# Kernel optimization log

Measured on AMD Instinct MI355X. Metric: run time of the kernel, lower is better.

## Reference

```python
import jax, jax.numpy as jnp
import numpy as np

TEMPERATURE = 0.07
EPS = 1e-12  # F.normalize clamp


def _project(x, We, be, W1, b1, W2, b2):
    # encoder Linear then projection head Linear->ReLU->Linear
    h = x @ We + be                      # [B, 512]
    h = jax.nn.relu(h @ W1 + b1)         # [B, 256]
    return h @ W2 + b2                   # [B, 128]


def _ntxent(z1, z2, t):
    B = z1.shape[0]
    z1 = z1 / jnp.maximum(jnp.linalg.norm(z1, axis=1, keepdims=True), EPS)
    z2 = z2 / jnp.maximum(jnp.linalg.norm(z2, axis=1, keepdims=True), EPS)
    reps = jnp.concatenate([z1, z2], axis=0)          # [2B, 128]
    sim = reps @ reps.T                               # [2B, 2B]
    N = 2 * B
    idx = jnp.arange(N)
    # positives: eye rolled by B along columns -> column (i+B) mod N
    pos = sim[idx, (idx + B) % N][:, None]            # [N, 1]
    # negatives: all off-diagonal entries per row, in column order
    cols = jnp.arange(N - 1)[None, :]                 # [1, N-1]
    neg_idx = cols + (cols >= idx[:, None])           # skip the diagonal
    neg = jnp.take_along_axis(sim, neg_idx, axis=1)   # [N, N-1]
    logits = jnp.concatenate([pos, neg], axis=1) / t  # [N, N]
    # cross-entropy with label 0
    return jnp.mean(jax.nn.logsumexp(logits, axis=1) - logits[:, 0])


def setup_inputs() -> dict:
    key = jax.random.key(0)
    ks = jax.random.split(key, 10)
    B, Din, Denc, Dh, Dp = 4096, 1024, 512, 256, 128
    s = lambda fan_in: 1.0 / np.sqrt(fan_in)
    return {
        "x_image": jax.random.normal(ks[0], (B, Din), jnp.float32),
        "x_text": jax.random.normal(ks[1], (B, Din), jnp.float32),
        "We_img": jax.random.normal(ks[2], (Din, Denc), jnp.float32) * s(Din),
        "be_img": jnp.zeros((Denc,), jnp.float32),
        "We_txt": jax.random.normal(ks[3], (Din, Denc), jnp.float32) * s(Din),
        "be_txt": jnp.zeros((Denc,), jnp.float32),
        "Wp1_img": jax.random.normal(ks[4], (Denc, Dh), jnp.float32) * s(Denc),
        "bp1_img": jnp.zeros((Dh,), jnp.float32),
        "Wp2_img": jax.random.normal(ks[5], (Dh, Dp), jnp.float32) * s(Dh),
        "bp2_img": jnp.zeros((Dp,), jnp.float32),
        "Wp1_txt": jax.random.normal(ks[6], (Denc, Dh), jnp.float32) * s(Denc),
        "bp1_txt": jnp.zeros((Dh,), jnp.float32),
        "Wp2_txt": jax.random.normal(ks[7], (Dh, Dp), jnp.float32) * s(Dh),
        "bp2_txt": jnp.zeros((Dp,), jnp.float32),
    }


def reference(x_image, x_text, We_img, be_img, We_txt, be_txt,
              Wp1_img, bp1_img, Wp2_img, bp2_img,
              Wp1_txt, bp1_txt, Wp2_txt, bp2_txt):
    z1 = _project(x_image, We_img, be_img, Wp1_img, bp1_img, Wp2_img, bp2_img)
    z2 = _project(x_text, We_txt, be_txt, Wp1_txt, bp1_txt, Wp2_txt, bp2_txt)
    # single modality pair ('image','text') -> one NT-Xent loss
    return _ntxent(z1, z2, TEMPERATURE)
```

## Files before the change

kernel.cpp:

```cpp
#include <hip/hip_runtime.h>
#include <hip/hip_bf16.h>
#include <math.h>

typedef __bf16 bf16_t;
typedef __bf16 bf8 __attribute__((ext_vector_type(8)));
typedef __bf16 bf4 __attribute__((ext_vector_type(4)));
typedef float f32x4 __attribute__((ext_vector_type(4)));
typedef int i32x8 __attribute__((ext_vector_type(8)));
typedef unsigned char u8;

#define AS1 __attribute__((address_space(1)))
#define AS3 __attribute__((address_space(3)))

#define B_ROWS 4096
#define NTOT   8192
#define DIN    1024
#define DENC   512
#define DH     256
#define DP     128
#define NSLICE 64
#define INV_T        14.285714285714286f
#define SCALE_LOG2   20.609929155556620f

__device__ __forceinline__ f32x4 mfma_16x16x32(bf8 a, bf8 b, f32x4 c) {
  return __builtin_amdgcn_mfma_f32_16x16x32_bf16(a, b, c, 0, 0, 0);
}

__global__ __launch_bounds__(256) void prep_kernel(
    const float* __restrict__ x_i, const float* __restrict__ x_t,
    const float* __restrict__ We_i, const float* __restrict__ We_t,
    const float* __restrict__ W1_i, const float* __restrict__ W1_t,
    const float* __restrict__ W2_i, const float* __restrict__ W2_t,
    bf16_t* __restrict__ xb_i, bf16_t* __restrict__ xb_t,
    bf16_t* __restrict__ Wet_i, bf16_t* __restrict__ Wet_t,
    bf16_t* __restrict__ W1t_i, bf16_t* __restrict__ W1t_t,
    bf16_t* __restrict__ W2t_i, bf16_t* __restrict__ W2t_t) {
  const int b = blockIdx.x;
  const int tid = threadIdx.x;
  if (b >= 336) {
    int idx = (b - 336) * 256 + tid;
    const int HALF = (B_ROWS * DIN) / 4;
    const float* s; bf16_t* d; int off;
    if (idx < HALF) { s = x_i; d = xb_i; off = idx; }
    else            { s = x_t; d = xb_t; off = idx - HALF; }
    float4 v = ((const float4*)s)[off];
    bf4 w = { (bf16_t)v.x, (bf16_t)v.y, (bf16_t)v.z, (bf16_t)v.w };
    ((bf4*)d)[off] = w;
    return;
  }
  const float* src; bf16_t* dst; int K, N, tile;
  if (b < 128)      { src = We_i; dst = Wet_i; K = 1024; N = 512; tile = b; }
  else if (b < 256) { src = We_t; dst = Wet_t; K = 1024; N = 512; tile = b - 128; }
  else if (b < 288) { src = W1_i; dst = W1t_i; K = 512;  N = 256; tile = b - 256; }
  else if (b < 320) { src = W1_t; dst = W1t_t; K = 512;  N = 256; tile = b - 288; }
  else if (b < 328) { src = W2_i; dst = W2t_i; K = 256;  N = 128; tile = b - 320; }
  else              { src = W2_t; dst = W2t_t; K = 256;  N = 128; tile = b - 328; }
  const int tilesN = N >> 6;
  const int k0 = (tile / tilesN) * 64;
  const int n0 = (tile % tilesN) * 64;

  __shared__ float ld[64][65];
  #pragma unroll
  for (int i = 0; i < 4; ++i) {
    int cid = tid + i * 256;
    int r = cid >> 4;
    int c = (cid & 15) * 4;
    float4 v = *(const float4*)(src + (size_t)(k0 + r) * N + n0 + c);
    ld[r][c + 0] = v.x; ld[r][c + 1] = v.y; ld[r][c + 2] = v.z; ld[r][c + 3] = v.w;
  }
  __syncthreads();
  #pragma unroll
  for (int i = 0; i < 2; ++i) {
    int cid = tid + i * 256;
    int rn = cid >> 3;
    int c8 = (cid & 7) * 8;
    bf8 w;
    #pragma unroll
    for (int j = 0; j < 8; ++j) w[j] = (bf16_t)ld[c8 + j][rn];
    *(bf8*)(dst + (size_t)(n0 + rn) * K + k0 + c8) = w;
  }
}

template<int MT, bool RELU>
__global__ __launch_bounds__(256) void gemm_glds(
    const bf16_t* __restrict__ A0, const bf16_t* __restrict__ A1,
    const bf16_t* __restrict__ B0, const bf16_t* __restrict__ B1,
    const float* __restrict__ bias0, const float* __restrict__ bias1,
    bf16_t* __restrict__ out0, bf16_t* __restrict__ out1,
    int N, int K) {
  const bf16_t* A   = blockIdx.z ? A1 : A0;
  const bf16_t* Bt  = blockIdx.z ? B1 : B0;
  const float* bias = blockIdx.z ? bias1 : bias0;
  bf16_t* outp      = blockIdx.z ? out1 : out0;

  const int nb   = blockIdx.x * 64;
  const int mb   = blockIdx.y * MT;
  const int tid  = threadIdx.x;
  const int wave = tid >> 6;
  const int lane = tid & 63;
  const int l15  = lane & 15;
  const int quad = lane >> 4;
  constexpr int CH = MT / 64;

  __shared__ __align__(16) bf16_t As[2][MT * 32];
  __shared__ __align__(16) bf16_t Bs[2][64 * 32];

  f32x4 acc[CH][4];
  #pragma unroll
  for (int i = 0; i < CH; ++i)
    #pragma unroll
    for (int j = 0; j < 4; ++j) acc[i][j] = (f32x4){0.f, 0.f, 0.f, 0.f};

  auto stage = [&](int k0, int pb) {
    #pragma unroll
    for (int i = 0; i < CH; ++i) {
      const int s = tid + i * 256;
      const bf16_t* ga = A + (size_t)(mb + (s >> 2)) * K + k0 + (s & 3) * 8;
      __builtin_amdgcn_global_load_lds(
          (const AS1 void*)ga,
          (AS3 void*)(As[pb] + (size_t)(wave * 64 + i * 256) * 8), 16, 0, 0);
    }
    const bf16_t* gb = Bt + (size_t)(nb + (tid >> 2)) * K + k0 + (tid & 3) * 8;
    __builtin_amdgcn_global_load_lds(
        (const AS1 void*)gb,
        (AS3 void*)(Bs[pb] + (size_t)(wave * 64) * 8), 16, 0, 0);
  };

  stage(0, 0);
  const int T = K >> 5;
  for (int t = 0; t < T; ++t) {
    __syncthreads();
    if (t + 1 < T) stage((t + 1) << 5, (t + 1) & 1);
    const bf16_t* as = As[t & 1];
    const bf16_t* bs = Bs[t & 1];
    bf8 a[CH];
    #pragma unroll
    for (int i = 0; i < CH; ++i)
      a[i] = *(const bf8*)(as + (size_t)(wave * (16 * CH) + i * 16 + l15) * 32 + quad * 8);
    #pragma unroll
    for (int nt = 0; nt < 4; ++nt) {
      bf8 bb = *(const bf8*)(bs + (size_t)(nt * 16 + l15) * 32 + quad * 8);
      #pragma unroll
      for (int i = 0; i < CH; ++i)
        acc[i][nt] = mfma_16x16x32(a[i], bb, acc[i][nt]);
    }
  }

  #pragma unroll
  for (int i = 0; i < CH; ++i) {
    const int orow = mb + wave * (16 * CH) + i * 16 + quad * 4;
    #pragma unroll
    for (int nt = 0; nt < 4; ++nt) {
      const int ocol = nb + nt * 16 + l15;
      const float bval = bias[ocol];
      #pragma unroll
      for (int r = 0; r < 4; ++r) {
        float v = acc[i][nt][r] + bval;
        if (RELU) v = fmaxf(v, 0.f);
        outp[(size_t)(orow + r) * N + ocol] = (bf16_t)v;
      }
    }
  }
}

__global__ __launch_bounds__(256) void head2_norm(
    const bf16_t* __restrict__ A0, const bf16_t* __restrict__ A1,
    const bf16_t* __restrict__ B0, const bf16_t* __restrict__ B1,
    const float* __restrict__ bias0, const float* __restrict__ bias1,
    u8* __restrict__ reps8) {
  const bf16_t* A   = blockIdx.z ? A1 : A0;
  const bf16_t* Bt  = blockIdx.z ? B1 : B0;
  const float* bias = blockIdx.z ? bias1 : bias0;

  const int mb   = blockIdx.x * 16;
  const int tid  = threadIdx.x;
  const int wave = tid >> 6;
  const int lane = tid & 63;
  const int l15  = lane & 15;
  const int quad = lane >> 4;
  const int wc0  = wave * 32;

  __shared__ __align__(16) bf16_t Asb[2][16 * 32];
  __shared__ __align__(16) bf16_t Bsb[2][128 * 32];
  __shared__ float ssL[64];

  f32x4 acc[2];
  acc[0] = (f32x4){0.f, 0.f, 0.f, 0.f};
  acc[1] = (f32x4){0.f, 0.f, 0.f, 0.f};

  auto stage = [&](int k0, int pb) {
    if (wave == 0) {
      const int row = lane >> 2, j = lane & 3, cf = j ^ (row & 3);
      const bf16_t* ga = A + (size_t)(mb + row) * DH + k0 + cf * 8;
      __builtin_amdgcn_global_load_lds(
          (const AS1 void*)ga, (AS3 void*)(Asb[pb]), 16, 0, 0);
    }
    #pragma unroll
    for (int i = 0; i < 2; ++i) {
      const int s = wave * 64 + i * 256 + lane;
      const int col = s >> 2, j = s & 3, cf = j ^ (col & 3);
      const bf16_t* gb = Bt + (size_t)col * DH + k0 + cf * 8;
      __builtin_amdgcn_global_load_lds(
          (const AS1 void*)gb,
          (AS3 void*)(Bsb[pb] + (size_t)(wave * 64 + i * 256) * 8), 16, 0, 0);
    }
  };

  stage(0, 0);
  for (int t = 0; t < 8; ++t) {
    __syncthreads();
    if (t < 7) stage((t + 1) << 5, (t + 1) & 1);
    const bf16_t* as = Asb[t & 1];
    const bf16_t* bs = Bsb[t & 1];
    bf8 a = *(const bf8*)(as + (size_t)(l15 * 4 + (quad ^ (l15 & 3))) * 8);
    #pragma unroll
    for (int nt = 0; nt < 2; ++nt) {
      const int col = wc0 + nt * 16 + l15;
      bf8 bb = *(const bf8*)(bs + (size_t)(col * 4 + (quad ^ (col & 3))) * 8);
      acc[nt] = mfma_16x16x32(a, bb, acc[nt]);
    }
  }

  float ssp[4];
  #pragma unroll
  for (int r = 0; r < 4; ++r) {
    #pragma unroll
    for (int nt = 0; nt < 2; ++nt) acc[nt][r] += bias[wc0 + nt * 16 + l15];
    float s = acc[0][r] * acc[0][r] + acc[1][r] * acc[1][r];
    s += __shfl_xor(s, 1); s += __shfl_xor(s, 2);
    s += __shfl_xor(s, 4); s += __shfl_xor(s, 8);
    ssp[r] = s;
  }
  if (l15 == 0) {
    #pragma unroll
    for (int r = 0; r < 4; ++r) ssL[wave * 16 + quad * 4 + r] = ssp[r];
  }
  __syncthreads();
  const size_t gr0 = (size_t)(blockIdx.z ? B_ROWS : 0) + mb + quad * 4;
  #pragma unroll
  for (int r = 0; r < 4; ++r) {
    const int row = quad * 4 + r;
    float tot = ssL[row] + ssL[16 + row] + ssL[32 + row] + ssL[48 + row];
    const float inv = 1.0f / fmaxf(sqrtf(tot), 1e-12f);
    int pk = __builtin_amdgcn_cvt_pk_fp8_f32(acc[0][r] * inv, acc[1][r] * inv, 0, 0);
    reps8[(gr0 + r) * DP + wc0 + l15]      = (u8)(pk & 0xff);
    reps8[(gr0 + r) * DP + wc0 + 16 + l15] = (u8)((pk >> 8) & 0xff);
  }
}

__global__ __launch_bounds__(256, 4) void sim_fp8_kernel(
    const u8* __restrict__ reps8, float* __restrict__ Spart) {
  const int l = blockIdx.x;
  int by = (int)((65.0f - sqrtf(4225.0f - 4.0f * (float)l)) * 0.5f);
  while ((by + 1) * (65 - (by + 1)) <= l) ++by;
  while (by * (65 - by) > l) --by;
  const int bxh = 2 * by + (l - by * (65 - by));
  const bool diag = (bxh - 2 * by) < 2;
  const int rowbase = by * 256;
  const int col0    = bxh * 128;
  const int tid  = threadIdx.x;
  const int wave = tid >> 6;
  const int lane = tid & 63;
  const int l15  = lane & 15;
  const int quad = lane >> 4;

  __shared__ __align__(16) u8 Bs[2][64 * DP];
  __shared__ float csw[4][128];

  const int r0 = rowbase + wave * 64;
  i32x8 af[4];
  #pragma unroll
  for (int c = 0; c < 4; ++c) {
    const uint4* ap = (const uint4*)(reps8 + (size_t)(r0 + c * 16 + l15) * DP + quad * 32);
    uint4 x0 = ap[0], x1 = ap[1];
    af[c] = (i32x8){(int)x0.x, (int)x0.y, (int)x0.z, (int)x0.w,
                    (int)x1.x, (int)x1.y, (int)x1.z, (int)x1.w};
  }

  float rs[4][4];
  #pragma unroll
  for (int c = 0; c < 4; ++c)
    #pragma unroll
    for (int r = 0; r < 4; ++r) rs[c][r] = 0.f;

  auto stage = [&](int t, int pb) {
    const int jt0 = col0 + t * 64;
    #pragma unroll
    for (int i = 0; i < 2; ++i) {
      const int s   = i * 256 + tid;
      const int col = s >> 3;
      const int cf  = (s & 7) ^ (col & 7);
      const u8* g = reps8 + (size_t)(jt0 + col) * DP + cf * 16;
      __builtin_amdgcn_global_load_lds(
          (const AS1 void*)g,
          (AS3 void*)(Bs[pb] + (size_t)(i * 256 + wave * 64) * 16), 16, 0, 0);
    }
  };

  stage(0, 0);
  for (int t = 0; t < 2; ++t) {
    __syncthreads();
    if (t == 0) stage(1, 1);
    const u8* buf = Bs[t & 1];

    #pragma unroll
    for (int g = 0; g < 2; ++g) {
      f32x4 pacc[2][4];
      __builtin_amdgcn_s_setprio(1);
      #pragma unroll
      for (int h = 0; h < 2; ++h) {
        const int st = g * 2 + h;
        const int coln = st * 16 + l15;
        const u8* cbase = buf + (size_t)coln * DP;
        const int c0 = ((2 * quad)     ^ (coln & 7)) * 16;
        const int c1 = ((2 * quad + 1) ^ (coln & 7)) * 16;
        uint4 b0 = *(const uint4*)(cbase + c0);
        uint4 b1 = *(const uint4*)(cbase + c1);
        i32x8 bf = (i32x8){(int)b0.x, (int)b0.y, (int)b0.z, (int)b0.w,
                           (int)b1.x, (int)b1.y, (int)b1.z, (int)b1.w};
        #pragma unroll
        for (int c = 0; c < 4; ++c) {
          pacc[h][c] = __builtin_amdgcn_mfma_scale_f32_16x16x128_f8f6f4(
              af[c], bf, (f32x4){0.f, 0.f, 0.f, 0.f}, 0, 0, 0,
              0x7F7F7F7F, 0, 0x7F7F7F7F);
        }
      }
      __builtin_amdgcn_s_setprio(0);

      #pragma unroll
      for (int h = 0; h < 2; ++h) {
        float csp[4] = {0.f, 0.f, 0.f, 0.f};
        #pragma unroll
        for (int c = 0; c < 4; ++c) {
          #pragma unroll
          for (int r = 0; r < 4; ++r) {
            float ev = __builtin_amdgcn_exp2f(pacc[h][c][r] * SCALE_LOG2);
            rs[c][r] += ev;
            csp[r] += ev;
          }
        }
        if (!diag) {
          float cs = (csp[0] + csp[1]) + (csp[2] + csp[3]);
          cs += __shfl_xor(cs, 16);
          cs += __shfl_xor(cs, 32);
          if (quad == 0) csw[wave][t * 64 + (g * 2 + h) * 16 + l15] = cs;
        }
      }
    }
  }

  #pragma unroll
  for (int c = 0; c < 4; ++c) {
    const int i0 = r0 + c * 16 + quad * 4;
    #pragma unroll
    for (int r = 0; r < 4; ++r) {
      float v = rs[c][r];
      v += __shfl_xor(v, 1); v += __shfl_xor(v, 2);
      v += __shfl_xor(v, 4); v += __shfl_xor(v, 8);
      if (l15 == 0) Spart[(size_t)bxh * NTOT + i0 + r] = v;
    }
  }

  if (!diag) {
    __syncthreads();
    if (tid < 128) {
      Spart[(size_t)(2 * by) * NTOT + col0 + tid] = csw[0][tid] + csw[1][tid];
    } else {
      const int j = tid - 128;
      Spart[(size_t)(2 * by + 1) * NTOT + col0 + j] = csw[2][j] + csw[3][j];
    }
  }
}

__global__ __launch_bounds__(256) void rowfinal_kernel(
    const u8* __restrict__ reps8, const float* __restrict__ Spart,
    float* __restrict__ L) {
  const int tid  = threadIdx.x;
  const int wave = tid >> 6;
  const int lane = tid & 63;
  const int row  = blockIdx.x * 4 + wave;
  const int ua = *(const unsigned short*)(reps8 + (size_t)row * DP + lane * 2);
  const int ub = *(const unsigned short*)(reps8 + (size_t)(row ^ B_ROWS) * DP + lane * 2);
  float a0 = __builtin_amdgcn_cvt_f32_fp8(ua, 0);
  float a1 = __builtin_amdgcn_cvt_f32_fp8(ua, 1);
  float b0 = __builtin_amdgcn_cvt_f32_fp8(ub, 0);
  float b1 = __builtin_amdgcn_cvt_f32_fp8(ub, 1);
  float dii = a0 * a0 + a1 * a1;
  float pos = a0 * b0 + a1 * b1;
  float ps  = Spart[(size_t)lane * NTOT + row];
  #pragma unroll
  for (int m = 1; m < 64; m <<= 1) {
    dii += __shfl_xor(dii, m);
    pos += __shfl_xor(pos, m);
    ps  += __shfl_xor(ps, m);
  }
  if (lane == 0) {
    float Si = ps - __builtin_amdgcn_exp2f(dii * SCALE_LOG2)
                  + __builtin_amdgcn_exp2f(pos * SCALE_LOG2);
    L[row] = logf(Si) - pos * INV_T;
  }
}

__global__ __launch_bounds__(1024) void reduce_kernel(
    const float* __restrict__ L, float* __restrict__ out) {
  const int tid = threadIdx.x;
  float acc = 0.f;
  for (int i = tid; i < NTOT; i += 1024) acc += L[i];
  #pragma unroll
  for (int m = 1; m < 64; m <<= 1) acc += __shfl_xor(acc, m);
  __shared__ float wsum[16];
  if ((tid & 63) == 0) wsum[tid >> 6] = acc;
  __syncthreads();
  if (tid < 16) {
    float v = wsum[tid];
    #pragma unroll
    for (int m = 1; m < 16; m <<= 1) v += __shfl_xor(v, m);
    if (tid == 0) out[0] = v * (1.0f / NTOT);
  }
}

extern "C" void kernel_launch(void* const* d_in, const int* in_sizes, int n_in,
                              void* d_out, int out_size, void* d_ws, size_t ws_size,
                              hipStream_t stream) {
  const float* x_img  = (const float*)d_in[0];
  const float* x_txt  = (const float*)d_in[1];
  const float* We_img = (const float*)d_in[2];
  const float* be_img = (const float*)d_in[3];
  const float* We_txt = (const float*)d_in[4];
  const float* be_txt = (const float*)d_in[5];
  const float* W1_img = (const float*)d_in[6];
  const float* b1_img = (const float*)d_in[7];
  const float* W2_img = (const float*)d_in[8];
  const float* b2_img = (const float*)d_in[9];
  const float* W1_txt = (const float*)d_in[10];
  const float* b1_txt = (const float*)d_in[11];
  const float* W2_txt = (const float*)d_in[12];
  const float* b2_txt = (const float*)d_in[13];

  char* p = (char*)d_ws;
  bf16_t* xbf_img = (bf16_t*)p; p += (size_t)B_ROWS * DIN * 2;
  bf16_t* xbf_txt = (bf16_t*)p; p += (size_t)B_ROWS * DIN * 2;
  bf16_t* Wet_img = (bf16_t*)p; p += (size_t)DENC * DIN * 2;
  bf16_t* Wet_txt = (bf16_t*)p; p += (size_t)DENC * DIN * 2;
  bf16_t* W1t_img = (bf16_t*)p; p += (size_t)DH * DENC * 2;
  bf16_t* W1t_txt = (bf16_t*)p; p += (size_t)DH * DENC * 2;
  bf16_t* W2t_img = (bf16_t*)p; p += (size_t)DP * DH * 2;
  bf16_t* W2t_txt = (bf16_t*)p; p += (size_t)DP * DH * 2;
  bf16_t* h_img   = (bf16_t*)p; p += (size_t)B_ROWS * DENC * 2;
  bf16_t* h_txt   = (bf16_t*)p; p += (size_t)B_ROWS * DENC * 2;
  bf16_t* g_img   = (bf16_t*)p; p += (size_t)B_ROWS * DH * 2;
  bf16_t* g_txt   = (bf16_t*)p; p += (size_t)B_ROWS * DH * 2;
  u8*     reps8   = (u8*)    p; p += (size_t)NTOT * DP;
  float*  Spart   = (float*) p; p += (size_t)NSLICE * NTOT * 4;
  float*  L       = (float*) p; p += (size_t)NTOT * 4;

  prep_kernel<<<336 + 8192, 256, 0, stream>>>(
      x_img, x_txt, We_img, We_txt, W1_img, W1_txt, W2_img, W2_txt,
      xbf_img, xbf_txt, Wet_img, Wet_txt, W1t_img, W1t_txt, W2t_img, W2t_txt);

  gemm_glds<128, false><<<dim3(DENC / 64, B_ROWS / 128, 2), 256, 0, stream>>>(
      xbf_img, xbf_txt, Wet_img, Wet_txt, be_img, be_txt, h_img, h_txt,
      DENC, DIN);
  gemm_glds<64, true><<<dim3(DH / 64, B_ROWS / 64, 2), 256, 0, stream>>>(
      h_img, h_txt, W1t_img, W1t_txt, b1_img, b1_txt, g_img, g_txt,
      DH, DENC);
  head2_norm<<<dim3(B_ROWS / 16, 1, 2), 256, 0, stream>>>(
      g_img, g_txt, W2t_img, W2t_txt, b2_img, b2_txt, reps8);

  sim_fp8_kernel<<<dim3(1056), 256, 0, stream>>>(reps8, Spart);
  rowfinal_kernel<<<NTOT / 4, 256, 0, stream>>>(reps8, Spart, L);
  reduce_kernel<<<1, 1024, 0, stream>>>(L, (float*)d_out);
}
```

Measured before the change: 182.7 us.

## Triple-buffer GEMM K-loop and preload whole head2 operands into LDS

The generic GEMM kernel moves from double to triple buffering. It uses explicit vmcnt waits and a raw s_barrier, so two tiles stay in flight while one is being computed, which is meant to hide global-to-LDS latency. head2_norm drops its staged K-loop and loads all 8 K-slices of A and B into LDS up front, then runs a fully unrolled MFMA loop with a single barrier. This costs more LDS per block (about 72KB for head2), which may lower occupancy, and the hand-counted vmcnt values must match the number of loads issued per stage.

```diff
diff --git a/kernel.cpp b/kernel.cpp
--- a/kernel.cpp
+++ b/kernel.cpp
@@ -102,8 +102,8 @@
   const int quad = lane >> 4;
   constexpr int CH = MT / 64;
 
-  __shared__ __align__(16) bf16_t As[2][MT * 32];
-  __shared__ __align__(16) bf16_t Bs[2][64 * 32];
+  __shared__ __align__(16) bf16_t As[3][MT * 32];
+  __shared__ __align__(16) bf16_t Bs[3][64 * 32];
 
   f32x4 acc[CH][4];
   #pragma unroll
@@ -126,13 +126,21 @@
         (AS3 void*)(Bs[pb] + (size_t)(wave * 64) * 8), 16, 0, 0);
   };
 
+  const int T = K >> 5;
   stage(0, 0);
-  const int T = K >> 5;
+  stage(32, 1);
   for (int t = 0; t < T; ++t) {
-    __syncthreads();
-    if (t + 1 < T) stage((t + 1) << 5, (t + 1) & 1);
-    const bf16_t* as = As[t & 1];
-    const bf16_t* bs = Bs[t & 1];
+    if (t == T - 1) {
+      asm volatile("s_waitcnt vmcnt(0)" ::: "memory");
+    } else if constexpr (CH == 2) {
+      asm volatile("s_waitcnt vmcnt(3)" ::: "memory");
+    } else {
+      asm volatile("s_waitcnt vmcnt(2)" ::: "memory");
+    }
+    __builtin_amdgcn_s_barrier();
+    if (t + 2 < T) stage((t + 2) << 5, (t + 2) % 3);
+    const bf16_t* as = As[t % 3];
+    const bf16_t* bs = Bs[t % 3];
     bf8 a[CH];
     #pragma unroll
     for (int i = 0; i < CH; ++i)
@@ -180,43 +188,44 @@
   const int quad = lane >> 4;
   const int wc0  = wave * 32;
 
-  __shared__ __align__(16) bf16_t Asb[2][16 * 32];
-  __shared__ __align__(16) bf16_t Bsb[2][128 * 32];
+  __shared__ __align__(16) bf16_t Asb[8 * 16 * 32];
+  __shared__ __align__(16) bf16_t Bsb[8 * 128 * 32];
   __shared__ float ssL[64];
+
+  #pragma unroll
+  for (int i = 0; i < 2; ++i) {
+    const int s = i * 256 + tid;
+    const int kt = s >> 6, slot = s & 63;
+    const int row = slot >> 2, j = slot & 3, cf = j ^ (row & 3);
+    const bf16_t* ga = A + (size_t)(mb + row) * DH + kt * 32 + cf * 8;
+    __builtin_amdgcn_global_load_lds(
+        (const AS1 void*)ga,
+        (AS3 void*)(Asb + (size_t)(i * 256 + wave * 64) * 8), 16, 0, 0);
+  }
+  #pragma unroll
+  for (int i = 0; i < 16; ++i) {
+    const int s2 = i * 256 + tid;
+    const int kt = s2 >> 9, slot = s2 & 511;
+    const int col = slot >> 2, j = slot & 3, cf = j ^ (col & 3);
+    const bf16_t* gb = Bt + (size_t)col * DH + kt * 32 + cf * 8;
+    __builtin_amdgcn_global_load_lds(
+        (const AS1 void*)gb,
+        (AS3 void*)(Bsb + (size_t)(i * 256 + wave * 64) * 8), 16, 0, 0);
+  }
+  __syncthreads();
 
   f32x4 acc[2];
   acc[0] = (f32x4){0.f, 0.f, 0.f, 0.f};
   acc[1] = (f32x4){0.f, 0.f, 0.f, 0.f};
-
-  auto stage = [&](int k0, int pb) {
-    if (wave == 0) {
-      const int row = lane >> 2, j = lane & 3, cf = j ^ (row & 3);
-      const bf16_t* ga = A + (size_t)(mb + row) * DH + k0 + cf * 8;
-      __builtin_amdgcn_global_load_lds(
-          (const AS1 void*)ga, (AS3 void*)(Asb[pb]), 16, 0, 0);
-    }
-    #pragma unroll
-    for (int i = 0; i < 2; ++i) {
-      const int s = wave * 64 + i * 256 + lane;
-      const int col = s >> 2, j = s & 3, cf = j ^ (col & 3);
-      const bf16_t* gb = Bt + (size_t)col * DH + k0 + cf * 8;
-      __builtin_amdgcn_global_load_lds(
-          (const AS1 void*)gb,
-          (AS3 void*)(Bsb[pb] + (size_t)(wave * 64 + i * 256) * 8), 16, 0, 0);
-    }
-  };
-
-  stage(0, 0);
-  for (int t = 0; t < 8; ++t) {
-    __syncthreads();
-    if (t < 7) stage((t + 1) << 5, (t + 1) & 1);
-    const bf16_t* as = Asb[t & 1];
-    const bf16_t* bs = Bsb[t & 1];
-    bf8 a = *(const bf8*)(as + (size_t)(l15 * 4 + (quad ^ (l15 & 3))) * 8);
+  #pragma unroll
+  for (int kt = 0; kt < 8; ++kt) {
+    bf8 a = *(const bf8*)(Asb + (size_t)kt * 512 +
+                          (size_t)(l15 * 4 + (quad ^ (l15 & 3))) * 8);
     #pragma unroll
     for (int nt = 0; nt < 2; ++nt) {
       const int col = wc0 + nt * 16 + l15;
-      bf8 bb = *(const bf8*)(bs + (size_t)(col * 4 + (quad ^ (col & 3))) * 8);
+      bf8 bb = *(const bf8*)(Bsb + (size_t)kt * 4096 +
+                             (size_t)(col * 4 + (quad ^ (col & 3))) * 8);
       acc[nt] = mfma_16x16x32(a, bb, acc[nt]);
     }
   }
```

Result: no change. 182.2 us (-0.3%).

## Fuse all stages into one persistent kernel with software grid barriers

Applied to the files above, without the earlier changes.

Replaces the seven-kernel pipeline (prep, two GEMMs, head+norm, fp8 similarity, row-final, reduce) with a single persistent kernel of 512 blocks. The stages are separated by atomic-counter grid barriers, and the final reduction goes through per-block partials. The GEMM tile loop also moves to a 3-stage LDS ring with explicit vmcnt waits in place of double buffering. The aim is to remove launch gaps and tail effects between kernels. In exchange it needs every block co-resident (a deadlock risk), adds a memset launch, and the fixed grid may load-balance stages like the 1056-tile similarity worse.

```diff
diff --git a/kernel.cpp b/kernel.cpp
--- a/kernel.cpp
+++ b/kernel.cpp
@@ -19,6 +19,7 @@
 #define DH     256
 #define DP     128
 #define NSLICE 64
+#define GRID   512
 #define INV_T        14.285714285714286f
 #define SCALE_LOG2   20.609929155556620f
 
@@ -26,84 +27,33 @@
   return __builtin_amdgcn_mfma_f32_16x16x32_bf16(a, b, c, 0, 0, 0);
 }
 
-__global__ __launch_bounds__(256) void prep_kernel(
-    const float* __restrict__ x_i, const float* __restrict__ x_t,
-    const float* __restrict__ We_i, const float* __restrict__ We_t,
-    const float* __restrict__ W1_i, const float* __restrict__ W1_t,
-    const float* __restrict__ W2_i, const float* __restrict__ W2_t,
-    bf16_t* __restrict__ xb_i, bf16_t* __restrict__ xb_t,
-    bf16_t* __restrict__ Wet_i, bf16_t* __restrict__ Wet_t,
-    bf16_t* __restrict__ W1t_i, bf16_t* __restrict__ W1t_t,
-    bf16_t* __restrict__ W2t_i, bf16_t* __restrict__ W2t_t) {
-  const int b = blockIdx.x;
-  const int tid = threadIdx.x;
-  if (b >= 336) {
-    int idx = (b - 336) * 256 + tid;
-    const int HALF = (B_ROWS * DIN) / 4;
-    const float* s; bf16_t* d; int off;
-    if (idx < HALF) { s = x_i; d = xb_i; off = idx; }
-    else            { s = x_t; d = xb_t; off = idx - HALF; }
-    float4 v = ((const float4*)s)[off];
-    bf4 w = { (bf16_t)v.x, (bf16_t)v.y, (bf16_t)v.z, (bf16_t)v.w };
-    ((bf4*)d)[off] = w;
-    return;
-  }
-  const float* src; bf16_t* dst; int K, N, tile;
-  if (b < 128)      { src = We_i; dst = Wet_i; K = 1024; N = 512; tile = b; }
-  else if (b < 256) { src = We_t; dst = Wet_t; K = 1024; N = 512; tile = b - 128; }
-  else if (b < 288) { src = W1_i; dst = W1t_i; K = 512;  N = 256; tile = b - 256; }
-  else if (b < 320) { src = W1_t; dst = W1t_t; K = 512;  N = 256; tile = b - 288; }
-  else if (b < 328) { src = W2_i; dst = W2t_i; K = 256;  N = 128; tile = b - 320; }
-  else              { src = W2_t; dst = W2t_t; K = 256;  N = 128; tile = b - 328; }
-  const int tilesN = N >> 6;
-  const int k0 = (tile / tilesN) * 64;
-  const int n0 = (tile % tilesN) * 64;
-
-  __shared__ float ld[64][65];
-  #pragma unroll
-  for (int i = 0; i < 4; ++i) {
-    int cid = tid + i * 256;
-    int r = cid >> 4;
-    int c = (cid & 15) * 4;
-    float4 v = *(const float4*)(src + (size_t)(k0 + r) * N + n0 + c);
-    ld[r][c + 0] = v.x; ld[r][c + 1] = v.y; ld[r][c + 2] = v.z; ld[r][c + 3] = v.w;
-  }
+__device__ __forceinline__ void grid_sync(unsigned* syncc, int slot) {
   __syncthreads();
-  #pragma unroll
-  for (int i = 0; i < 2; ++i) {
-    int cid = tid + i * 256;
-    int rn = cid >> 3;
-    int c8 = (cid & 7) * 8;
-    bf8 w;
-    #pragma unroll
-    for (int j = 0; j < 8; ++j) w[j] = (bf16_t)ld[c8 + j][rn];
-    *(bf8*)(dst + (size_t)(n0 + rn) * K + k0 + c8) = w;
-  }
+  if (threadIdx.x == 0) {
+    __builtin_amdgcn_fence(__ATOMIC_RELEASE, "agent");
+    __hip_atomic_fetch_add(&syncc[slot * 16], 1u, __ATOMIC_RELAXED,
+                           __HIP_MEMORY_SCOPE_AGENT);
+    while (__hip_atomic_load(&syncc[slot * 16], __ATOMIC_RELAXED,
+                             __HIP_MEMORY_SCOPE_AGENT) < (unsigned)GRID) {}
+    __builtin_amdgcn_fence(__ATOMIC_ACQUIRE, "agent");
+  }
+  __syncthreads();
 }
 
 template<int MT, bool RELU>
-__global__ __launch_bounds__(256) void gemm_glds(
-    const bf16_t* __restrict__ A0, const bf16_t* __restrict__ A1,
-    const bf16_t* __restrict__ B0, const bf16_t* __restrict__ B1,
-    const float* __restrict__ bias0, const float* __restrict__ bias1,
-    bf16_t* __restrict__ out0, bf16_t* __restrict__ out1,
-    int N, int K) {
-  const bf16_t* A   = blockIdx.z ? A1 : A0;
-  const bf16_t* Bt  = blockIdx.z ? B1 : B0;
-  const float* bias = blockIdx.z ? bias1 : bias0;
-  bf16_t* outp      = blockIdx.z ? out1 : out0;
-
-  const int nb   = blockIdx.x * 64;
-  const int mb   = blockIdx.y * MT;
+__device__ __forceinline__ void gemm_tile(
+    const bf16_t* A, const bf16_t* Bt, const float* bias, bf16_t* outp,
+    int N, int K, int nb, int mb, char* base) {
   const int tid  = threadIdx.x;
   const int wave = tid >> 6;
   const int lane = tid & 63;
   const int l15  = lane & 15;
   const int quad = lane >> 4;
-  constexpr int CH = MT / 64;
-
-  __shared__ __align__(16) bf16_t As[2][MT * 32];
-  __shared__ __align__(16) bf16_t Bs[2][64 * 32];
+  constexpr int CH  = MT / 64;
+  constexpr int ASZ = MT * 32;
+  constexpr int BSZ = 64 * 32;
+  bf16_t* As = (bf16_t*)base;
+  bf16_t* Bs = (bf16_t*)(base + (size_t)3 * ASZ * 2);
 
   f32x4 acc[CH][4];
   #pragma unroll
@@ -118,21 +68,29 @@
       const bf16_t* ga = A + (size_t)(mb + (s >> 2)) * K + k0 + (s & 3) * 8;
       __builtin_amdgcn_global_load_lds(
           (const AS1 void*)ga,
-          (AS3 void*)(As[pb] + (size_t)(wave * 64 + i * 256) * 8), 16, 0, 0);
+          (AS3 void*)(As + (size_t)pb * ASZ + (size_t)(wave * 64 + i * 256) * 8),
+          16, 0, 0);
     }
     const bf16_t* gb = Bt + (size_t)(nb + (tid >> 2)) * K + k0 + (tid & 3) * 8;
     __builtin_amdgcn_global_load_lds(
         (const AS1 void*)gb,
-        (AS3 void*)(Bs[pb] + (size_t)(wave * 64) * 8), 16, 0, 0);
+        (AS3 void*)(Bs + (size_t)pb * BSZ + (size_t)(wave * 64) * 8), 16, 0, 0);
   };
 
+  const int T = K >> 5;
   stage(0, 0);
-  const int T = K >> 5;
+  stage(32, 1);
   for (int t = 0; t < T; ++t) {
-    __syncthreads();
-    if (t + 1 < T) stage((t + 1) << 5, (t + 1) & 1);
-    const bf16_t* as = As[t & 1];
-    const bf16_t* bs = Bs[t & 1];
+    if (t == T - 1) {
+      asm volatile("s_waitcnt vmcnt(0)" ::: "memory");
+    } else {
+      if constexpr (CH == 2) asm volatile("s_waitcnt vmcnt(3)" ::: "memory");
+      else                   asm volatile("s_waitcnt vmcnt(2)" ::: "memory");
+    }
+    __builtin_amdgcn_s_barrier();
+    if (t + 2 < T) stage((t + 2) << 5, (t + 2) % 3);
+    const bf16_t* as = As + (size_t)(t % 3) * ASZ;
+    const bf16_t* bs = Bs + (size_t)(t % 3) * BSZ;
     bf8 a[CH];
     #pragma unroll
     for (int i = 0; i < CH; ++i)
@@ -163,259 +121,329 @@
   }
 }
 
-__global__ __launch_bounds__(256) void head2_norm(
-    const bf16_t* __restrict__ A0, const bf16_t* __restrict__ A1,
-    const bf16_t* __restrict__ B0, const bf16_t* __restrict__ B1,
-    const float* __restrict__ bias0, const float* __restrict__ bias1,
-    u8* __restrict__ reps8) {
-  const bf16_t* A   = blockIdx.z ? A1 : A0;
-  const bf16_t* Bt  = blockIdx.z ? B1 : B0;
-  const float* bias = blockIdx.z ? bias1 : bias0;
-
-  const int mb   = blockIdx.x * 16;
+__global__ __launch_bounds__(256, 2) void fused_all(
+    const float* x_i, const float* x_t,
+    const float* We_i, const float* We_t,
+    const float* W1_i, const float* W1_t,
+    const float* W2_i, const float* W2_t,
+    const float* be_i, const float* be_t,
+    const float* b1_i, const float* b1_t,
+    const float* b2_i, const float* b2_t,
+    bf16_t* xb_i, bf16_t* xb_t,
+    bf16_t* Wet_i, bf16_t* Wet_t,
+    bf16_t* W1t_i, bf16_t* W1t_t,
+    bf16_t* W2t_i, bf16_t* W2t_t,
+    bf16_t* h_i, bf16_t* h_t,
+    bf16_t* g_i, bf16_t* g_t,
+    u8* reps8, float* Spart,
+    float* partials, unsigned* syncc,
+    float* out) {
+  __shared__ __align__(16) char smem[36864];
+  const int bid  = blockIdx.x;
   const int tid  = threadIdx.x;
   const int wave = tid >> 6;
   const int lane = tid & 63;
   const int l15  = lane & 15;
   const int quad = lane >> 4;
-  const int wc0  = wave * 32;
-
-  __shared__ __align__(16) bf16_t Asb[2][16 * 32];
-  __shared__ __align__(16) bf16_t Bsb[2][128 * 32];
-  __shared__ float ssL[64];
-
-  f32x4 acc[2];
-  acc[0] = (f32x4){0.f, 0.f, 0.f, 0.f};
-  acc[1] = (f32x4){0.f, 0.f, 0.f, 0.f};
-
-  auto stage = [&](int k0, int pb) {
-    if (wave == 0) {
-      const int row = lane >> 2, j = lane & 3, cf = j ^ (row & 3);
-      const bf16_t* ga = A + (size_t)(mb + row) * DH + k0 + cf * 8;
-      __builtin_amdgcn_global_load_lds(
-          (const AS1 void*)ga, (AS3 void*)(Asb[pb]), 16, 0, 0);
-    }
-    #pragma unroll
-    for (int i = 0; i < 2; ++i) {
-      const int s = wave * 64 + i * 256 + lane;
-      const int col = s >> 2, j = s & 3, cf = j ^ (col & 3);
-      const bf16_t* gb = Bt + (size_t)col * DH + k0 + cf * 8;
-      __builtin_amdgcn_global_load_lds(
-          (const AS1 void*)gb,
-          (AS3 void*)(Bsb[pb] + (size_t)(wave * 64 + i * 256) * 8), 16, 0, 0);
-    }
-  };
-
-  stage(0, 0);
-  for (int t = 0; t < 8; ++t) {
+
+  for (int b = bid; b < 8528; b += GRID) {
+    if (b >= 336) {
+      int idx = (b - 336) * 256 + tid;
+      const int HALF = (B_ROWS * DIN) / 4;
+      const float* s; bf16_t* d; int off;
+      if (idx < HALF) { s = x_i; d = xb_i; off = idx; }
+      else            { s = x_t; d = xb_t; off = idx - HALF; }
+      float4 v = ((const float4*)s)[off];
+      bf4 w = { (bf16_t)v.x, (bf16_t)v.y, (bf16_t)v.z, (bf16_t)v.w };
+      ((bf4*)d)[off] = w;
+    } else {
+      const float* src; bf16_t* dst; int K, N, tile;
+      if (b < 128)      { src = We_i; dst = Wet_i; K = 1024; N = 512; tile = b; }
+      else if (b < 256) { src = We_t; dst = Wet_t; K = 1024; N = 512; tile = b - 128; }
+      else if (b < 288) { src = W1_i; dst = W1t_i; K = 512;  N = 256; tile = b - 256; }
+      else if (b < 320) { src = W1_t; dst = W1t_t; K = 512;  N = 256; tile = b - 288; }
+      else if (b < 328) { src = W2_i; dst = W2t_i; K = 256;  N = 128; tile = b - 320; }
+      else              { src = W2_t; dst = W2t_t; K = 256;  N = 128; tile = b - 328; }
+      const int tilesN = N >> 6;
+      const int k0 = (tile / tilesN) * 64;
+      const int n0 = (tile % tilesN) * 64;
+      float (*ld)[65] = (float(*)[65])smem;
+      #pragma unroll
+      for (int i = 0; i < 4; ++i) {
+        int cid = tid + i * 256;
+        int r = cid >> 4;
+        int c = (cid & 15) * 4;
+        float4 v = *(const float4*)(src + (size_t)(k0 + r) * N + n0 + c);
+        ld[r][c + 0] = v.x; ld[r][c + 1] = v.y; ld[r][c + 2] = v.z; ld[r][c + 3] = v.w;
+      }
+      __syncthreads();
+      #pragma unroll
+      for (int i = 0; i < 2; ++i) {
+        int cid = tid + i * 256;
+        int rn = cid >> 3;
+        int c8 = (cid & 7) * 8;
+        bf8 w;
+        #pragma unroll
+        for (int j = 0; j < 8; ++j) w[j] = (bf16_t)ld[c8 + j][rn];
+        *(bf8*)(dst + (size_t)(n0 + rn) * K + k0 + c8) = w;
+      }
+    }
+  }
+  grid_sync(syncc, 0);
+
+  {
+    const int nbi = bid & 7, mbi = (bid >> 3) & 31, z = bid >> 8;
+    gemm_tile<128, false>(z ? xb_t : xb_i, z ? Wet_t : Wet_i,
+                          z ? be_t : be_i, z ? h_t : h_i,
+                          DENC, DIN, nbi * 64, mbi * 128, smem);
+  }
+  grid_sync(syncc, 1);
+
+  {
+    const int nbi = bid & 3, mbi = (bid >> 2) & 63, z = bid >> 8;
+    gemm_tile<64, true>(z ? h_t : h_i, z ? W1t_t : W1t_i,
+                        z ? b1_t : b1_i, z ? g_t : g_i,
+                        DH, DENC, nbi * 64, mbi * 64, smem);
+  }
+  grid_sync(syncc, 2);
+
+  {
+    const int z = bid >> 8;
+    const int mb = (bid & 255) * 16;
+    const bf16_t* A    = z ? g_t : g_i;
+    const bf16_t* Bt   = z ? W2t_t : W2t_i;
+    const float*  bias = z ? b2_t : b2_i;
+    bf16_t* Asb = (bf16_t*)smem;
+    bf16_t* Bsb = (bf16_t*)(smem + 2048);
+    float*  ssL = (float*)(smem + 2048 + 16384);
+    const int wc0 = wave * 32;
+
+    f32x4 acc2[2];
+    acc2[0] = (f32x4){0.f, 0.f, 0.f, 0.f};
+    acc2[1] = (f32x4){0.f, 0.f, 0.f, 0.f};
+
+    auto stageh = [&](int k0, int pb) {
+      if (wave == 0) {
+        const int row = lane >> 2, j = lane & 3, cf = j ^ (row & 3);
+        const bf16_t* ga = A + (size_t)(mb + row) * DH + k0 + cf * 8;
+        __builtin_amdgcn_global_load_lds(
+            (const AS1 void*)ga, (AS3 void*)(Asb + (size_t)pb * 512), 16, 0, 0);
+      }
+      #pragma unroll
+      for (int i = 0; i < 2; ++i) {
+        const int s = wave * 64 + i * 256 + lane;
+        const int col = s >> 2, j = s & 3, cf = j ^ (col & 3);
+        const bf16_t* gb = Bt + (size_t)col * DH + k0 + cf * 8;
+        __builtin_amdgcn_global_load_lds(
+            (const AS1 void*)gb,
+            (AS3 void*)(Bsb + (size_t)pb * 4096 + (size_t)(wave * 64 + i * 256) * 8),
+            16, 0, 0);
+      }
+    };
+
+    stageh(0, 0);
+    for (int t = 0; t < 8; ++t) {
+      __syncthreads();
+      if (t < 7) stageh((t + 1) << 5, (t + 1) & 1);
+      const bf16_t* as = Asb + (size_t)(t & 1) * 512;
+      const bf16_t* bs = Bsb + (size_t)(t & 1) * 4096;
+      bf8 a = *(const bf8*)(as + (size_t)(l15 * 4 + (quad ^ (l15 & 3))) * 8);
+      #pragma unroll
+      for (int nt = 0; nt < 2; ++nt) {
+        const int col = wc0 + nt * 16 + l15;
+        bf8 bb = *(const bf8*)(bs + (size_t)(col * 4 + (quad ^ (col & 3))) * 8);
+        acc2[nt] = mfma_16x16x32(a, bb, acc2[nt]);
+      }
+    }
+
+    float ssp[4];
+    #pragma unroll
+    for (int r = 0; r < 4; ++r) {
+      #pragma unroll
+      for (int nt = 0; nt < 2; ++nt) acc2[nt][r] += bias[wc0 + nt * 16 + l15];
+      float s = acc2[0][r] * acc2[0][r] + acc2[1][r] * acc2[1][r];
+      s += __shfl_xor(s, 1); s += __shfl_xor(s, 2);
+      s += __shfl_xor(s, 4); s += __shfl_xor(s, 8);
+      ssp[r] = s;
+    }
+    if (l15 == 0) {
+      #pragma unroll
+      for (int r = 0; r < 4; ++r) ssL[wave * 16 + quad * 4 + r] = ssp[r];
+    }
     __syncthreads();
-    if (t < 7) stage((t + 1) << 5, (t + 1) & 1);
-    const bf16_t* as = Asb[t & 1];
-    const bf16_t* bs = Bsb[t & 1];
-    bf8 a = *(const bf8*)(as + (size_t)(l15 * 4 + (quad ^ (l15 & 3))) * 8);
-    #pragma unroll
-    for (int nt = 0; nt < 2; ++nt) {
-      const int col = wc0 + nt * 16 + l15;
-      bf8 bb = *(const bf8*)(bs + (size_t)(col * 4 + (quad ^ (col & 3))) * 8);
-      acc[nt] = mfma_16x16x32(a, bb, acc[nt]);
-    }
-  }
-
-  float ssp[4];
-  #pragma unroll
-  for (int r = 0; r < 4; ++r) {
-    #pragma unroll
-    for (int nt = 0; nt < 2; ++nt) acc[nt][r] += bias[wc0 + nt * 16 + l15];
-    float s = acc[0][r] * acc[0][r] + acc[1][r] * acc[1][r];
-    s += __shfl_xor(s, 1); s += __shfl_xor(s, 2);
-    s += __shfl_xor(s, 4); s += __shfl_xor(s, 8);
-    ssp[r] = s;
-  }
-  if (l15 == 0) {
-    #pragma unroll
-    for (int r = 0; r < 4; ++r) ssL[wave * 16 + quad * 4 + r] = ssp[r];
-  }
-  __syncthreads();
-  const size_t gr0 = (size_t)(blockIdx.z ? B_ROWS : 0) + mb + quad * 4;
-  #pragma unroll
-  for (int r = 0; r < 4; ++r) {
-    const int row = quad * 4 + r;
-    float tot = ssL[row] + ssL[16 + row] + ssL[32 + row] + ssL[48 + row];
-    const float inv = 1.0f / fmaxf(sqrtf(tot), 1e-12f);
-    int pk = __builtin_amdgcn_cvt_pk_fp8_f32(acc[0][r] * inv, acc[1][r] * inv, 0, 0);
-    reps8[(gr0 + r) * DP + wc0 + l15]      = (u8)(pk & 0xff);
-    reps8[(gr0 + r) * DP + wc0 + 16 + l15] = (u8)((pk >> 8) & 0xff);
-  }
-}
-
-__global__ __launch_bounds__(256, 4) void sim_fp8_kernel(
-    const u8* __restrict__ reps8, float* __restrict__ Spart) {
-  const int l = blockIdx.x;
-  int by = (int)((65.0f - sqrtf(4225.0f - 4.0f * (float)l)) * 0.5f);
-  while ((by + 1) * (65 - (by + 1)) <= l) ++by;
-  while (by * (65 - by) > l) --by;
-  const int bxh = 2 * by + (l - by * (65 - by));
-  const bool diag = (bxh - 2 * by) < 2;
-  const int rowbase = by * 256;
-  const int col0    = bxh * 128;
-  const int tid  = threadIdx.x;
-  const int wave = tid >> 6;
-  const int lane = tid & 63;
-  const int l15  = lane & 15;
-  const int quad = lane >> 4;
-
-  __shared__ __align__(16) u8 Bs[2][64 * DP];
-  __shared__ float csw[4][128];
-
-  const int r0 = rowbase + wave * 64;
-  i32x8 af[4];
-  #pragma unroll
-  for (int c = 0; c < 4; ++c) {
-    const uint4* ap = (const uint4*)(reps8 + (size_t)(r0 + c * 16 + l15) * DP + quad * 32);
-    uint4 x0 = ap[0], x1 = ap[1];
-    af[c] = (i32x8){(int)x0.x, (int)x0.y, (int)x0.z, (int)x0.w,
-                    (int)x1.x, (int)x1.y, (int)x1.z, (int)x1.w};
-  }
-
-  float rs[4][4];
-  #pragma unroll
-  for (int c = 0; c < 4; ++c)
-    #pragma unroll
-    for (int r = 0; r < 4; ++r) rs[c][r] = 0.f;
-
-  auto stage = [&](int t, int pb) {
-    const int jt0 = col0 + t * 64;
-    #pragma unroll
-    for (int i = 0; i < 2; ++i) {
-      const int s   = i * 256 + tid;
-      const int col = s >> 3;
-      const int cf  = (s & 7) ^ (col & 7);
-      const u8* g = reps8 + (size_t)(jt0 + col) * DP + cf * 16;
-      __builtin_amdgcn_global_load_lds(
-          (const AS1 void*)g,
-          (AS3 void*)(Bs[pb] + (size_t)(i * 256 + wave * 64) * 16), 16, 0, 0);
-    }
-  };
-
-  stage(0, 0);
-  for (int t = 0; t < 2; ++t) {
-    __syncthreads();
-    if (t == 0) stage(1, 1);
-    const u8* buf = Bs[t & 1];
-
-    #pragma unroll
-    for (int g = 0; g < 2; ++g) {
-      f32x4 pacc[2][4];
-      __builtin_amdgcn_s_setprio(1);
-      #pragma unroll
-      for (int h = 0; h < 2; ++h) {
-        const int st = g * 2 + h;
-        const int coln = st * 16 + l15;
-        const u8* cbase = buf + (size_t)coln * DP;
-        const int c0 = ((2 * quad)     ^ (coln & 7)) * 16;
-        const int c1 = ((2 * quad + 1) ^ (coln & 7)) * 16;
-        uint4 b0 = *(const uint4*)(cbase + c0);
-        uint4 b1 = *(const uint4*)(cbase + c1);
-        i32x8 bf = (i32x8){(int)b0.x, (int)b0.y, (int)b0.z, (int)b0.w,
-                           (int)b1.x, (int)b1.y, (int)b1.z, (int)b1.w};
+    const size_t gr0 = (size_t)(z ? B_ROWS : 0) + mb + quad * 4;
+    #pragma unroll
+    for (int r = 0; r < 4; ++r) {
+      const int row = quad * 4 + r;
+      float tot = ssL[row] + ssL[16 + row] + ssL[32 + row] + ssL[48 + row];
+      const float inv = 1.0f / fmaxf(sqrtf(tot), 1e-12f);
+      int pk = __builtin_amdgcn_cvt_pk_fp8_f32(acc2[0][r] * inv, acc2[1][r] * inv, 0, 0);
+      reps8[(gr0 + r) * DP + wc0 + l15]      = (u8)(pk & 0xff);
+      reps8[(gr0 + r) * DP + wc0 + 16 + l15] = (u8)((pk >> 8) & 0xff);
+    }
+  }
+  grid_sync(syncc, 3);
+
+  for (int ll = bid; ll < 1056; ll += GRID) {
+    int by = (int)((65.0f - sqrtf(4225.0f - 4.0f * (float)ll)) * 0.5f);
+    while ((by + 1) * (65 - (by + 1)) <= ll) ++by;
+    while (by * (65 - by) > ll) --by;
+    const int bxh = 2 * by + (ll - by * (65 - by));
+    const bool diag = (bxh - 2 * by) < 2;
+    const int rowbase = by * 256;
+    const int col0    = bxh * 128;
+
+    u8*    Bs8 = (u8*)smem;
+    float* csw = (float*)(smem + 16384);
+
+    const int r0 = rowbase + wave * 64;
+    i32x8 af[4];
+    #pragma unroll
+    for (int c = 0; c < 4; ++c) {
+      const uint4* ap = (const uint4*)(reps8 + (size_t)(r0 + c * 16 + l15) * DP + quad * 32);
+      uint4 x0 = ap[0], x1 = ap[1];
+      af[c] = (i32x8){(int)x0.x, (int)x0.y, (int)x0.z, (int)x0.w,
+                      (int)x1.x, (int)x1.y, (int)x1.z, (int)x1.w};
+    }
+
+    float rs[4][4];
+    #pragma unroll
+    for (int c = 0; c < 4; ++c)
+      #pragma unroll
+      for (int r = 0; r < 4; ++r) rs[c][r] = 0.f;
+
+    auto stage_s = [&](int t, int pb) {
+      const int jt0 = col0 + t * 64;
+      #pragma unroll
+      for (int i = 0; i < 2; ++i) {
+        const int s   = i * 256 + tid;
+        const int col = s >> 3;
+        const int cf  = (s & 7) ^ (col & 7);
+        const u8* g = reps8 + (size_t)(jt0 + col) * DP + cf * 16;
+        __builtin_amdgcn_global_load_lds(
+            (const AS1 void*)g,
+            (AS3 void*)(Bs8 + (size_t)pb * 8192 + (size_t)(i * 256 + wave * 64) * 16),
+            16, 0, 0);
+      }
+    };
+
+    stage_s(0, 0);
+    for (int t = 0; t < 2; ++t) {
+      __syncthreads();
+      if (t == 0) stage_s(1, 1);
+      const u8* buf = Bs8 + (size_t)(t & 1) * 8192;
+
+      #pragma unroll
+      for (int g = 0; g < 2; ++g) {
+        f32x4 pacc[2][4];
+        __builtin_amdgcn_s_setprio(1);
         #pragma unroll
-        for (int c = 0; c < 4; ++c) {
-          pacc[h][c] = __builtin_amdgcn_mfma_scale_f32_16x16x128_f8f6f4(
-              af[c], bf, (f32x4){0.f, 0.f, 0.f, 0.f}, 0, 0, 0,
-              0x7F7F7F7F, 0, 0x7F7F7F7F);
-        }
-      }
-      __builtin_amdgcn_s_setprio(0);
-
-      #pragma unroll
-      for (int h = 0; h < 2; ++h) {
-        float csp[4] = {0.f, 0.f, 0.f, 0.f};
-        #pragma unroll
-        for (int c = 0; c < 4; ++c) {
+        for (int h = 0; h < 2; ++h) {
+          const int st = g * 2 + h;
+          const int coln = st * 16 + l15;
+          const u8* cbase = buf + (size_t)coln * DP;
+          const int c0 = ((2 * quad)     ^ (coln & 7)) * 16;
+          const int c1 = ((2 * quad + 1) ^ (coln & 7)) * 16;
+          uint4 b0 = *(const uint4*)(cbase + c0);
+          uint4 b1 = *(const uint4*)(cbase + c1);
+          i32x8 bf = (i32x8){(int)b0.x, (int)b0.y, (int)b0.z, (int)b0.w,
+                             (int)b1.x, (int)b1.y, (int)b1.z, (int)b1.w};
           #pragma unroll
-          for (int r = 0; r < 4; ++r) {
-            float ev = __builtin_amdgcn_exp2f(pacc[h][c][r] * SCALE_LOG2);
-            rs[c][r] += ev;
-            csp[r] += ev;
+          for (int c = 0; c < 4; ++c) {
+            pacc[h][c] = __builtin_amdgcn_mfma_scale_f32_16x16x128_f8f6f4(
+                af[c], bf, (f32x4){0.f, 0.f, 0.f, 0.f}, 0, 0, 0,
+                0x7F7F7F7F, 0, 0x7F7F7F7F);
           }
         }
-        if (!diag) {
-          float cs = (csp[0] + csp[1]) + (csp[2] + csp[3]);
-          cs += __shfl_xor(cs, 16);
-          cs += __shfl_xor(cs, 32);
-          if (quad == 0) csw[wave][t * 64 + (g * 2 + h) * 16 + l15] = cs;
+        __builtin_amdgcn_s_setprio(0);
+
+        #pragma unroll
+        for (int h = 0; h < 2; ++h) {
+          float csp[4] = {0.f, 0.f, 0.f, 0.f};
+          #pragma unroll
+          for (int c = 0; c < 4; ++c) {
+            #pragma unroll
+            for (int r = 0; r < 4; ++r) {
+              float ev = __builtin_amdgcn_exp2f(pacc[h][c][r] * SCALE_LOG2);
+              rs[c][r] += ev;
+              csp[r] += ev;
+            }
+          }
+          if (!diag) {
+            float cs = (csp[0] + csp[1]) + (csp[2] + csp[3]);
+            cs += __shfl_xor(cs, 16);
+            cs += __shfl_xor(cs, 32);
+            if (quad == 0) csw[wave * 128 + t * 64 + (g * 2 + h) * 16 + l15] = cs;
+          }
         }
       }
     }
-  }
-
-  #pragma unroll
-  for (int c = 0; c < 4; ++c) {
-    const int i0 = r0 + c * 16 + quad * 4;
-    #pragma unroll
-    for (int r = 0; r < 4; ++r) {
-      float v = rs[c][r];
-      v += __shfl_xor(v, 1); v += __shfl_xor(v, 2);
-      v += __shfl_xor(v, 4); v += __shfl_xor(v, 8);
-      if (l15 == 0) Spart[(size_t)bxh * NTOT + i0 + r] = v;
-    }
-  }
-
-  if (!diag) {
+
+    #pragma unroll
+    for (int c = 0; c < 4; ++c) {
+      const int i0 = r0 + c * 16 + quad * 4;
+      #pragma unroll
+      for (int r = 0; r < 4; ++r) {
+        float v = rs[c][r];
+        v += __shfl_xor(v, 1); v += __shfl_xor(v, 2);
+        v += __shfl_xor(v, 4); v += __shfl_xor(v, 8);
+        if (l15 == 0) Spart[(size_t)bxh * NTOT + i0 + r] = v;
+      }
+    }
+
+    if (!diag) {
+      __syncthreads();
+      if (tid < 128) {
+        Spart[(size_t)(2 * by) * NTOT + col0 + tid] = csw[0 * 128 + tid] + csw[1 * 128 + tid];
+      } else {
+        const int j = tid - 128;
+        Spart[(size_t)(2 * by + 1) * NTOT + col0 + j] = csw[2 * 128 + j] + csw[3 * 128 + j];
+      }
+    }
+  }
+  grid_sync(syncc, 4);
+
+  {
+    float lsum = 0.f;
+    for (int u = bid; u < 2048; u += GRID) {
+      const int row = u * 4 + wave;
+      const int ua = *(const unsigned short*)(reps8 + (size_t)row * DP + lane * 2);
+      const int ub = *(const unsigned short*)(reps8 + (size_t)(row ^ B_ROWS) * DP + lane * 2);
+      float a0 = __builtin_amdgcn_cvt_f32_fp8(ua, 0);
+      float a1 = __builtin_amdgcn_cvt_f32_fp8(ua, 1);
+      float b0 = __builtin_amdgcn_cvt_f32_fp8(ub, 0);
+      float b1 = __builtin_amdgcn_cvt_f32_fp8(ub, 1);
+      float dii = a0 * a0 + a1 * a1;
+      float pos = a0 * b0 + a1 * b1;
+      float ps  = Spart[(size_t)lane * NTOT + row];
+      #pragma unroll
+      for (int m = 1; m < 64; m <<= 1) {
+        dii += __shfl_xor(dii, m);
+        pos += __shfl_xor(pos, m);
+        ps  += __shfl_xor(ps, m);
+      }
+      if (lane == 0) {
+        float Si = ps - __builtin_amdgcn_exp2f(dii * SCALE_LOG2)
+                      + __builtin_amdgcn_exp2f(pos * SCALE_LOG2);
+        lsum += logf(Si) - pos * INV_T;
+      }
+    }
     __syncthreads();
-    if (tid < 128) {
-      Spart[(size_t)(2 * by) * NTOT + col0 + tid] = csw[0][tid] + csw[1][tid];
-    } else {
-      const int j = tid - 128;
-      Spart[(size_t)(2 * by + 1) * NTOT + col0 + j] = csw[2][j] + csw[3][j];
-    }
-  }
-}
-
-__global__ __launch_bounds__(256) void rowfinal_kernel(
-    const u8* __restrict__ reps8, const float* __restrict__ Spart,
-    float* __restrict__ L) {
-  const int tid  = threadIdx.x;
-  const int wave = tid >> 6;
-  const int lane = tid & 63;
-  const int row  = blockIdx.x * 4 + wave;
-  const int ua = *(const unsigned short*)(reps8 + (size_t)row * DP + lane * 2);
-  const int ub = *(const unsigned short*)(reps8 + (size_t)(row ^ B_ROWS) * DP + lane * 2);
-  float a0 = __builtin_amdgcn_cvt_f32_fp8(ua, 0);
-  float a1 = __builtin_amdgcn_cvt_f32_fp8(ua, 1);
-  float b0 = __builtin_amdgcn_cvt_f32_fp8(ub, 0);
-  float b1 = __builtin_amdgcn_cvt_f32_fp8(ub, 1);
-  float dii = a0 * a0 + a1 * a1;
-  float pos = a0 * b0 + a1 * b1;
-  float ps  = Spart[(size_t)lane * NTOT + row];
-  #pragma unroll
-  for (int m = 1; m < 64; m <<= 1) {
-    dii += __shfl_xor(dii, m);
-    pos += __shfl_xor(pos, m);
-    ps  += __shfl_xor(ps, m);
-  }
-  if (lane == 0) {
-    float Si = ps - __builtin_amdgcn_exp2f(dii * SCALE_LOG2)
-                  + __builtin_amdgcn_exp2f(pos * SCALE_LOG2);
-    L[row] = logf(Si) - pos * INV_T;
-  }
-}
-
-__global__ __launch_bounds__(1024) void reduce_kernel(
-    const float* __restrict__ L, float* __restrict__ out) {
-  const int tid = threadIdx.x;
-  float acc = 0.f;
-  for (int i = tid; i < NTOT; i += 1024) acc += L[i];
-  #pragma unroll
-  for (int m = 1; m < 64; m <<= 1) acc += __shfl_xor(acc, m);
-  __shared__ float wsum[16];
-  if ((tid & 63) == 0) wsum[tid >> 6] = acc;
-  __syncthreads();
-  if (tid < 16) {
-    float v = wsum[tid];
-    #pragma unroll
-    for (int m = 1; m < 16; m <<= 1) v += __shfl_xor(v, m);
-    if (tid == 0) out[0] = v * (1.0f / NTOT);
+    float* ws = (float*)smem;
+    if (lane == 0) ws[wave] = lsum;
+    __syncthreads();
+    if (tid == 0) partials[bid] = ws[0] + ws[1] + ws[2] + ws[3];
+  }
+  grid_sync(syncc, 5);
+
+  if (bid == 0) {
+    float v = partials[tid] + partials[tid + 256];
+    #pragma unroll
+    for (int m = 1; m < 64; m <<= 1) v += __shfl_xor(v, m);
+    float* ws = (float*)smem;
+    if (lane == 0) ws[wave] = v;
+    __syncthreads();
+    if (tid == 0) out[0] = (ws[0] + ws[1] + ws[2] + ws[3]) * (1.0f / NTOT);
   }
 }
 
@@ -452,22 +480,14 @@
   bf16_t* g_txt   = (bf16_t*)p; p += (size_t)B_ROWS * DH * 2;
   u8*     reps8   = (u8*)    p; p += (size_t)NTOT * DP;
   float*  Spart   = (float*) p; p += (size_t)NSLICE * NTOT * 4;
-  float*  L       = (float*) p; p += (size_t)NTOT * 4;
-
-  prep_kernel<<<336 + 8192, 256, 0, stream>>>(
+  float*  partials= (float*) p; p += (size_t)GRID * 4;
+  unsigned* syncc = (unsigned*)p; p += 1024;
+
+  hipMemsetAsync((void*)syncc, 0, 1024, stream);
+  fused_all<<<GRID, 256, 0, stream>>>(
       x_img, x_txt, We_img, We_txt, W1_img, W1_txt, W2_img, W2_txt,
-      xbf_img, xbf_txt, Wet_img, Wet_txt, W1t_img, W1t_txt, W2t_img, W2t_txt);
-
-  gemm_glds<128, false><<<dim3(DENC / 64, B_ROWS / 128, 2), 256, 0, stream>>>(
-      xbf_img, xbf_txt, Wet_img, Wet_txt, be_img, be_txt, h_img, h_txt,
-      DENC, DIN);
-  gemm_glds<64, true><<<dim3(DH / 64, B_ROWS / 64, 2), 256, 0, stream>>>(
-      h_img, h_txt, W1t_img, W1t_txt, b1_img, b1_txt, g_img, g_txt,
-      DH, DENC);
-  head2_norm<<<dim3(B_ROWS / 16, 1, 2), 256, 0, stream>>>(
-      g_img, g_txt, W2t_img, W2t_txt, b2_img, b2_txt, reps8);
-
-  sim_fp8_kernel<<<dim3(1056), 256, 0, stream>>>(reps8, Spart);
-  rowfinal_kernel<<<NTOT / 4, 256, 0, stream>>>(reps8, Spart, L);
-  reduce_kernel<<<1, 1024, 0, stream>>>(L, (float*)d_out);
+      be_img, be_txt, b1_img, b1_txt, b2_img, b2_txt,
+      xbf_img, xbf_txt, Wet_img, Wet_txt, W1t_img, W1t_txt, W2t_img, W2t_txt,
+      h_img, h_txt, g_img, g_txt, reps8, Spart, partials, syncc,
+      (float*)d_out);
 }
```

Result: slower. 391.9 us (+114.5%).
